# Performance work log

Hardware: AMD Instinct MI355X
Metric: run time of the kernel (lower is better)

The kernel has to match this reference:

```python
import jax, jax.numpy as jnp
import numpy as np

VOL = (32, 64, 64)          # 3D brain volume grid
B, N, D = 2, 4096, 1024     # batch, active voxels (seq_len), feature_dim
H, KNN = 16, 16             # num_heads, num_neighbors


def setup_inputs() -> dict:
    key = jax.random.key(0)
    k1, k2, k3, k4 = jax.random.split(key, 4)
    # boolean 3D mask with exactly N active voxels (so seq_len == #active)
    rng = np.random.default_rng(0)
    flat = np.zeros(int(np.prod(VOL)), dtype=bool)
    flat[rng.choice(flat.size, N, replace=False)] = True
    visual_cortex_mask = jnp.asarray(flat.reshape(VOL))
    x = jax.random.normal(k1, (B, N, D), dtype=jnp.float32)
    s = 1.0 / np.sqrt(D)
    Wq = jax.random.normal(k2, (D, D), dtype=jnp.float32) * s
    Wk = jax.random.normal(k3, (D, D), dtype=jnp.float32) * s
    Wv = jax.random.normal(k4, (D, D), dtype=jnp.float32) * s
    return {"x": x, "visual_cortex_mask": visual_cortex_mask,
            "Wq": Wq, "Wk": Wk, "Wv": Wv}


def reference(x, visual_cortex_mask, Wq, Wk, Wv):
    batch, seq_len, d = x.shape
    hd = d // H
    # --- kNN over active voxel coordinates (cdist + topk) ---
    flat = visual_cortex_mask.reshape(-1)
    (act,) = jnp.nonzero(flat, size=seq_len)  # flat indices of active voxels
    coords = jnp.stack(jnp.unravel_index(act, visual_cortex_mask.shape),
                       axis=1).astype(jnp.float32)           # [N, 3]
    sq = jnp.sum(coords * coords, axis=-1)                    # [N]
    d2 = sq[:, None] + sq[None, :] - 2.0 * (coords @ coords.T)  # squared dists
    _, nbr = jax.lax.top_k(-d2, KNN + 1)   # smallest distances first
    nbr = nbr[:, 1:]                       # drop self -> [N, KNN] positions
    # --- QKV projections (torch Linear: x @ W.T) ---
    q = (x @ Wq.T).reshape(batch, seq_len, H, hd)
    k = (x @ Wk.T).reshape(batch, seq_len, H, hd)
    v = (x @ Wv.T).reshape(batch, seq_len, H, hd)
    # --- gather-based sparse attention: each query attends only to its
    # KNN neighbors (exactly the block-mask semantics of the original) ---
    kn = k[:, nbr]   # [B, N, KNN, H, hd]
    vn = v[:, nbr]   # [B, N, KNN, H, hd]
    scale = 1.0 / np.sqrt(hd)
    scores = jnp.einsum('bnhd,bnkhd->bhnk', q, kn) * scale
    attn = jax.nn.softmax(scores, axis=-1)
    out = jnp.einsum('bhnk,bnkhd->bnhd', attn, vn).reshape(batch, seq_len, d)
    metric = k.mean(axis=2)  # key.mean over heads -> [B, N, hd]
    return out, metric
```

## Files before the change

### kernel.cpp

```cpp
#include <hip/hip_runtime.h>
#include <hip/hip_bf16.h>
#include <stdint.h>

#define BATCH 2
#define NPTS 4096
#define DMODEL 1024
#define NHEAD 16
#define HDIM 64
#define KNN 16
#define MASKN 131072
#define EBLK 128

typedef __attribute__((ext_vector_type(8))) short bf16x8;
typedef __attribute__((ext_vector_type(4))) float f32x4;

__device__ __forceinline__ float b2f(unsigned short u) {
    union { unsigned int i; float f; } c; c.i = ((unsigned int)u) << 16; return c.f;
}
__device__ __forceinline__ unsigned short f2b(float f) {
    unsigned int x = __float_as_uint(f);
    unsigned int r = (x + 0x7fffu + ((x >> 16) & 1u)) >> 16;
    return (unsigned short)r;
}
__device__ __forceinline__ unsigned int pack2f(float a, float b) {
    return (unsigned int)f2b(a) | ((unsigned int)f2b(b) << 16);
}
__device__ __forceinline__ void gload16(const unsigned short* g, unsigned short* l) {
    __builtin_amdgcn_global_load_lds((const __attribute__((address_space(1))) void*)g,
                                     (__attribute__((address_space(3))) void*)l, 16, 0, 0);
}

__global__ __launch_bounds__(256) void count8_kernel(const unsigned char* __restrict__ m8,
                                                     int* __restrict__ cnt8) {
    __shared__ int red[256];
    const int b = blockIdx.x, t = threadIdx.x;
    const uchar4 v = ((const uchar4*)m8)[b * 256 + t];
    red[t] = (v.x != 0) + (v.y != 0) + (v.z != 0) + (v.w != 0);
    __syncthreads();
    for (int off = 128; off >= 1; off >>= 1) {
        if (t < off) red[t] += red[t + off];
        __syncthreads();
    }
    if (t == 0) cnt8[b] = red[0];
}

__global__ __launch_bounds__(256) void count32_kernel(const unsigned char* __restrict__ m8,
                                                      const int* __restrict__ cnt8,
                                                      int* __restrict__ cnt32) {
    __shared__ int red[256];
    const int b = blockIdx.x, t = threadIdx.x;
    red[t] = (t < EBLK) ? cnt8[t] : 0;
    __syncthreads();
    for (int off = 128; off >= 1; off >>= 1) {
        if (t < off) red[t] += red[t + off];
        __syncthreads();
    }
    if (red[0] == NPTS) return;
    __syncthreads();
    const int4 v = ((const int4*)m8)[b * 256 + t];
    red[t] = (v.x != 0) + (v.y != 0) + (v.z != 0) + (v.w != 0);
    __syncthreads();
    for (int off = 128; off >= 1; off >>= 1) {
        if (t < off) red[t] += red[t + off];
        __syncthreads();
    }
    if (t == 0) cnt32[b] = red[0];
}

__global__ __launch_bounds__(256) void extract_kernel(const unsigned char* __restrict__ m8,
                                                      const int* __restrict__ cnt8,
                                                      const int* __restrict__ cnt32,
                                                      int* __restrict__ act) {
    __shared__ int sblk[EBLK];
    __shared__ int sthr[256];
    const int b = blockIdx.x, t = threadIdx.x;
    if (t < EBLK) sblk[t] = cnt8[t];
    __syncthreads();
    for (int off = 1; off < EBLK; off <<= 1) {
        int v = (t < EBLK && t >= off) ? sblk[t - off] : 0;
        __syncthreads();
        if (t < EBLK) sblk[t] += v;
        __syncthreads();
    }
    const bool bytes = (sblk[EBLK - 1] == NPTS);
    if (!bytes) {
        __syncthreads();
        if (t < EBLK) sblk[t] = cnt32[t];
        __syncthreads();
        for (int off = 1; off < EBLK; off <<= 1) {
            int v = (t < EBLK && t >= off) ? sblk[t - off] : 0;
            __syncthreads();
            if (t < EBLK) sblk[t] += v;
            __syncthreads();
        }
    }
    const int blkoff = (b == 0) ? 0 : sblk[b - 1];
    const int gbase = b * 1024 + t * 4;
    int f0, f1, f2, f3;
    if (bytes) {
        const uchar4 v = ((const uchar4*)m8)[b * 256 + t];
        f0 = v.x != 0; f1 = v.y != 0; f2 = v.z != 0; f3 = v.w != 0;
    } else {
        const int4 v = ((const int4*)m8)[b * 256 + t];
        f0 = v.x != 0; f1 = v.y != 0; f2 = v.z != 0; f3 = v.w != 0;
    }
    const int c = f0 + f1 + f2 + f3;
    sthr[t] = c;
    __syncthreads();
    for (int off = 1; off < 256; off <<= 1) {
        int v = (t >= off) ? sthr[t - off] : 0;
        __syncthreads();
        sthr[t] += v;
        __syncthreads();
    }
    int pos = blkoff + sthr[t] - c;
    if (f0) act[pos++] = gbase;
    if (f1) act[pos++] = gbase + 1;
    if (f2) act[pos++] = gbase + 2;
    if (f3) act[pos++] = gbase + 3;
}

__global__ __launch_bounds__(256) void knn_kernel(const int* __restrict__ act,
                                                  int* __restrict__ nbr) {
    __shared__ int act_s[NPTS];
    const int t = threadIdx.x;
    for (int i = t; i < NPTS; i += 256) act_s[i] = act[i];
    __syncthreads();
    const int q = blockIdx.x * 4 + (t >> 6);
    const int lane = t & 63;
    const int aq = act_s[q];
    const int qz = aq >> 12, qy = (aq >> 6) & 63, qx = aq & 63;
    int best[17];
    #pragma unroll
    for (int i = 0; i < 17; ++i) best[i] = 0x7FFFFFFF;
    for (int j = lane; j < NPTS; j += 64) {
        const int aj = act_s[j];
        const int dz = (aj >> 12) - qz;
        const int dy = ((aj >> 6) & 63) - qy;
        const int dx = (aj & 63) - qx;
        const int d2 = dz * dz + dy * dy + dx * dx;
        int p = (d2 << 12) | j;
        if (p < best[16]) {
            #pragma unroll
            for (int u = 0; u < 17; ++u) {
                const bool lt = p < best[u];
                const int tmp = best[u];
                best[u] = lt ? p : best[u];
                p = lt ? tmp : p;
            }
        }
    }
    int head = best[0];
    int keep = 0;
    #pragma unroll
    for (int r = 0; r < KNN + 1; ++r) {
        int m = head;
        #pragma unroll
        for (int off = 32; off >= 1; off >>= 1) m = min(m, __shfl_xor(m, off, 64));
        if (lane == r - 1) keep = m;
        const bool win = (head == m);
        #pragma unroll
        for (int u = 0; u < 16; ++u) if (win) best[u] = best[u + 1];
        if (win) best[16] = 0x7FFFFFFF;
        head = best[0];
    }
    if (lane < KNN) nbr[q * KNN + lane] = keep & 4095;
}

#define XN8 (BATCH * NPTS * DMODEL / 8)
#define WN8 (DMODEL * DMODEL / 8)
__global__ __launch_bounds__(256) void cast_all_kernel(
    const float* __restrict__ x, const float* __restrict__ wq,
    const float* __restrict__ wk, const float* __restrict__ wv,
    unsigned short* __restrict__ Xb, unsigned short* __restrict__ Wb) {
    const int i = blockIdx.x * 256 + threadIdx.x;
    const int total = XN8 + 3 * WN8;
    if (i >= total) return;
    const float* src;
    unsigned short* dst;
    if (i < XN8) {
        src = x + (size_t)i * 8;
        dst = Xb + (size_t)i * 8;
    } else {
        const int j = i - XN8;
        const int wsel = j >> 17;
        const int o = j & (WN8 - 1);
        src = ((wsel == 0) ? wq : (wsel == 1) ? wk : wv) + (size_t)o * 8;
        dst = Wb + ((size_t)wsel * WN8 + o) * 8;
    }
    const float4 a = ((const float4*)src)[0];
    const float4 b = ((const float4*)src)[1];
    uint4 w;
    w.x = pack2f(a.x, a.y); w.y = pack2f(a.z, a.w);
    w.z = pack2f(b.x, b.y); w.w = pack2f(b.z, b.w);
    *(uint4*)dst = w;
}

__global__ __launch_bounds__(256, 2) void gemm_qkv3(
    const unsigned short* __restrict__ Xb,
    const unsigned short* __restrict__ Wb,
    unsigned short* __restrict__ O0, unsigned short* __restrict__ O1, unsigned short* __restrict__ O2)
{
    const int K = DMODEL, N = DMODEL;
    __shared__ unsigned short As[2][128 * 32];
    __shared__ unsigned short Bs[3][2][128 * 32];
    const int tid = threadIdx.x;
    const int rowBase = blockIdx.x * 128;
    const int colBase = blockIdx.y * 128;
    const int lane = tid & 63, w = tid >> 6;
    const int wr = w >> 1, wc = w & 1;
    const int lr = lane & 15, kg = lane >> 4;

    f32x4 acc[3][4][4];
    const f32x4 zero = {0.f, 0.f, 0.f, 0.f};
    #pragma unroll
    for (int z = 0; z < 3; ++z)
        #pragma unroll
        for (int i = 0; i < 4; ++i)
            #pragma unroll
            for (int j = 0; j < 4; ++j) acc[z][i][j] = zero;

    const int srow4 = tid >> 2;
    const int xch = (tid & 3) ^ (srow4 & 3);
    const unsigned short* agp = &Xb[(size_t)(rowBase + srow4) * K + xch * 8];
    const unsigned short* bg0 = &Wb[(size_t)(colBase + srow4) * K + xch * 8];
    const unsigned short* bg1 = bg0 + (size_t)DMODEL * DMODEL;
    const unsigned short* bg2 = bg1 + (size_t)DMODEL * DMODEL;

    #define STAGE(kt, bf) do { \
        gload16(agp + (kt) * 32,           &As[bf][w * 512]); \
        gload16(agp + 64 * K + (kt) * 32,  &As[bf][2048 + w * 512]); \
        gload16(bg0 + (kt) * 32,           &Bs[0][bf][w * 512]); \
        gload16(bg0 + 64 * K + (kt) * 32,  &Bs[0][bf][2048 + w * 512]); \
        gload16(bg1 + (kt) * 32,           &Bs[1][bf][w * 512]); \
        gload16(bg1 + 64 * K + (kt) * 32,  &Bs[1][bf][2048 + w * 512]); \
        gload16(bg2 + (kt) * 32,           &Bs[2][bf][w * 512]); \
        gload16(bg2 + 64 * K + (kt) * 32,  &Bs[2][bf][2048 + w * 512]); \
    } while (0)

    const int rchunk = (kg ^ (lr & 3)) * 8;

    #define COMPUTE(bf) do { \
        bf16x8 af[4]; \
        _Pragma("unroll") \
        for (int mi = 0; mi < 4; ++mi) \
            af[mi] = *(const bf16x8*)&As[bf][(wr * 64 + mi * 16 + lr) * 32 + rchunk]; \
        _Pragma("unroll") \
        for (int z = 0; z < 3; ++z) { \
            bf16x8 bfr[4]; \
            _Pragma("unroll") \
            for (int ni = 0; ni < 4; ++ni) \
                bfr[ni] = *(const bf16x8*)&Bs[z][bf][(wc * 64 + ni * 16 + lr) * 32 + rchunk]; \
            __builtin_amdgcn_s_setprio(1); \
            _Pragma("unroll") \
            for (int mi = 0; mi < 4; ++mi) \
                _Pragma("unroll") \
                for (int ni = 0; ni < 4; ++ni) \
                    acc[z][mi][ni] = __builtin_amdgcn_mfma_f32_16x16x32_bf16(af[mi], bfr[ni], acc[z][mi][ni], 0, 0, 0); \
            __builtin_amdgcn_s_setprio(0); \
        } \
    } while (0)

    STAGE(0, 0);
    STAGE(1, 1);
    for (int kt = 0; kt < 30; ++kt) {
        const int bf = kt & 1;
        asm volatile("s_waitcnt vmcnt(8)" ::: "memory");
        __builtin_amdgcn_s_barrier();
        COMPUTE(bf);
        __builtin_amdgcn_s_barrier();
        STAGE(kt + 2, bf);
    }
    asm volatile("s_waitcnt vmcnt(8)" ::: "memory");
    __builtin_amdgcn_s_barrier();
    COMPUTE(0);
    __builtin_amdgcn_s_barrier();
    asm volatile("s_waitcnt vmcnt(0)" ::: "memory");
    __builtin_amdgcn_s_barrier();
    COMPUTE(1);
    #undef STAGE
    #undef COMPUTE

    #pragma unroll
    for (int z = 0; z < 3; ++z) {
        unsigned short* C = (z == 0) ? O0 : (z == 1) ? O1 : O2;
        #pragma unroll
        for (int mi = 0; mi < 4; ++mi)
            #pragma unroll
            for (int ni = 0; ni < 4; ++ni) {
                const int row0 = rowBase + wr * 64 + mi * 16 + kg * 4;
                const int col = colBase + wc * 64 + ni * 16 + lr;
                #pragma unroll
                for (int j = 0; j < 4; ++j)
                    C[(size_t)(row0 + j) * N + col] = f2b(acc[z][mi][ni][j]);
            }
    }
}

__device__ __forceinline__ void stage16(unsigned short* dst, const float* src) {
    const float4 a = ((const float4*)src)[0];
    const float4 b = ((const float4*)src)[1];
    const float4 c = ((const float4*)src)[2];
    const float4 d = ((const float4*)src)[3];
    uint4 w0, w1;
    w0.x = pack2f(a.x, a.y); w0.y = pack2f(a.z, a.w);
    w0.z = pack2f(b.x, b.y); w0.w = pack2f(b.z, b.w);
    w1.x = pack2f(c.x, c.y); w1.y = pack2f(c.z, c.w);
    w1.z = pack2f(d.x, d.y); w1.w = pack2f(d.z, d.w);
    ((uint4*)dst)[0] = w0;
    ((uint4*)dst)[1] = w1;
}

__global__ __launch_bounds__(256) void gemm_qkv_f32(
    const float* __restrict__ X,
    const float* __restrict__ W0, const float* __restrict__ W1, const float* __restrict__ W2,
    unsigned short* __restrict__ O0, unsigned short* __restrict__ O1, unsigned short* __restrict__ O2)
{
    const int K = DMODEL, N = DMODEL;
    const float* W = (blockIdx.z == 0) ? W0 : (blockIdx.z == 1) ? W1 : W2;
    unsigned short* C = (blockIdx.z == 0) ? O0 : (blockIdx.z == 1) ? O1 : O2;
    __shared__ unsigned short As[128 * 32];
    __shared__ unsigned short Bs[128 * 32];
    const int tid = threadIdx.x;
    const int rowBase = blockIdx.x * 128;
    const int colBase = blockIdx.y * 128;
    const int lane = tid & 63, w = tid >> 6;
    const int wr = w >> 1, wc = w & 1;
    const int lr = lane & 15, kg = lane >> 4;
    const int srow = tid >> 1;
    const int scol = (tid & 1) * 16;
    f32x4 acc[4][4];
    const f32x4 zero = {0.f, 0.f, 0.f, 0.f};
    #pragma unroll
    for (int i = 0; i < 4; ++i)
        #pragma unroll
        for (int j = 0; j < 4; ++j) acc[i][j] = zero;
    const float* Arow = &X[(size_t)(rowBase + srow) * K + scol];
    const float* Brow = &W[(size_t)(colBase + srow) * K + scol];
    unsigned short* Adst = &As[srow * 32 + scol];
    unsigned short* Bdst = &Bs[srow * 32 + scol];
    for (int kb = 0; kb < K; kb += 32) {
        __syncthreads();
        stage16(Adst, Arow + kb);
        stage16(Bdst, Brow + kb);
        __syncthreads();
        bf16x8 af[4], bfr[4];
        #pragma unroll
        for (int mi = 0; mi < 4; ++mi)
            af[mi] = *(const bf16x8*)&As[(wr * 64 + mi * 16 + lr) * 32 + kg * 8];
        #pragma unroll
        for (int ni = 0; ni < 4; ++ni)
            bfr[ni] = *(const bf16x8*)&Bs[(wc * 64 + ni * 16 + lr) * 32 + kg * 8];
        #pragma unroll
        for (int mi = 0; mi < 4; ++mi)
            #pragma unroll
            for (int ni = 0; ni < 4; ++ni)
                acc[mi][ni] = __builtin_amdgcn_mfma_f32_16x16x32_bf16(af[mi], bfr[ni], acc[mi][ni], 0, 0, 0);
    }
    #pragma unroll
    for (int mi = 0; mi < 4; ++mi)
        #pragma unroll
        for (int ni = 0; ni < 4; ++ni) {
            const int row0 = rowBase + wr * 64 + mi * 16 + kg * 4;
            const int col = colBase + wc * 64 + ni * 16 + lr;
            #pragma unroll
            for (int j = 0; j < 4; ++j)
                C[(size_t)(row0 + j) * N + col] = f2b(acc[mi][ni][j]);
        }
}

__global__ __launch_bounds__(256) void attn_kernel(
    const unsigned short* __restrict__ Q, const unsigned short* __restrict__ Kb,
    const unsigned short* __restrict__ Vb, const int* __restrict__ nbr,
    float* __restrict__ out, float* __restrict__ mout)
{
    const int bid = blockIdx.x;
    const int p = (bid & 7) * 1024 + (bid >> 3);
    const int b = p >> 12;
    const int n = p & 4095;
    __shared__ unsigned short q_s[DMODEL];
    __shared__ float a_s[NHEAD][KNN];
    __shared__ float part_s[4][64];
    const int tid = threadIdx.x;
    const int kk = tid & 15, h = tid >> 4;
    const int mynb = nbr[n * KNN + kk];
    const unsigned short* krow = &Kb[((size_t)b * NPTS + mynb) * DMODEL + h * HDIM];
    bf16x8 kreg[8];
    #pragma unroll
    for (int j = 0; j < 8; ++j) kreg[j] = *(const bf16x8*)&krow[j * 8];
    const int o = tid * 4;
    ushort4 vpre[KNN];
    #pragma unroll
    for (int k2 = 0; k2 < KNN; ++k2) {
        const int nb2 = __shfl(mynb, k2, 16);
        vpre[k2] = *(const ushort4*)&Vb[((size_t)b * NPTS + nb2) * DMODEL + o];
    }
    *(int2*)&q_s[tid * 4] = *(const int2*)&Q[((size_t)b * NPTS + n) * DMODEL + tid * 4];
    __syncthreads();
    float s = 0.f;
    #pragma unroll
    for (int j = 0; j < 8; ++j) {
        const bf16x8 qq = *(const bf16x8*)&q_s[h * HDIM + j * 8];
        const bf16x8 kr = kreg[j];
        #pragma unroll
        for (int e = 0; e < 8; ++e)
            s += b2f((unsigned short)qq[e]) * b2f((unsigned short)kr[e]);
    }
    s *= 0.125f;
    float m = s;
    #pragma unroll
    for (int off = 8; off >= 1; off >>= 1) m = fmaxf(m, __shfl_xor(m, off, 16));
    const float e = __expf(s - m);
    float sum = e;
    #pragma unroll
    for (int off = 8; off >= 1; off >>= 1) sum += __shfl_xor(sum, off, 16);
    a_s[h][kk] = e / sum;
    __syncthreads();
    const int h2 = tid >> 4;
    float av0 = 0.f, av1 = 0.f, av2 = 0.f, av3 = 0.f;
    #pragma unroll
    for (int k2 = 0; k2 < KNN; ++k2) {
        const float a = a_s[h2][k2];
        av0 += a * b2f(vpre[k2].x); av1 += a * b2f(vpre[k2].y);
        av2 += a * b2f(vpre[k2].z); av3 += a * b2f(vpre[k2].w);
    }
    float4 r; r.x = av0; r.y = av1; r.z = av2; r.w = av3;
    *(float4*)&out[((size_t)b * NPTS + n) * DMODEL + o] = r;
    {
        const unsigned short* krow2 = &Kb[((size_t)b * NPTS + n) * DMODEL];
        const int dd = tid & 63, grp = tid >> 6;
        float ms = 0.f;
        #pragma unroll
        for (int hh = 0; hh < 4; ++hh)
            ms += b2f(krow2[(grp * 4 + hh) * HDIM + dd]);
        part_s[grp][dd] = ms;
        __syncthreads();
        if (tid < 64)
            mout[((size_t)b * NPTS + n) * HDIM + tid] =
                (part_s[0][tid] + part_s[1][tid] + part_s[2][tid] + part_s[3][tid]) * 0.0625f;
    }
}

extern "C" void kernel_launch(void* const* d_in, const int* in_sizes, int n_in,
                              void* d_out, int out_size, void* d_ws, size_t ws_size,
                              hipStream_t stream) {
    const float* x = (const float*)d_in[0];
    const unsigned char* mask = (const unsigned char*)d_in[1];
    const float* Wq = (const float*)d_in[2];
    const float* Wk = (const float*)d_in[3];
    const float* Wv = (const float*)d_in[4];
    float* out = (float*)d_out;
    char* ws = (char*)d_ws;

    const size_t QKV_BYTES = (size_t)BATCH * NPTS * DMODEL * 2;
    const size_t XB_BYTES  = (size_t)BATCH * NPTS * DMODEL * 2;
    const size_t WB_BYTES  = (size_t)3 * DMODEL * DMODEL * 2;
    unsigned short* qb = (unsigned short*)(ws);
    unsigned short* kb = (unsigned short*)(ws + QKV_BYTES);
    unsigned short* vb = (unsigned short*)(ws + 2 * QKV_BYTES);
    const size_t SMALL_BYTES = (size_t)NPTS * sizeof(int) * (1 + KNN) + 2 * EBLK * sizeof(int);
    const size_t need_base = 3 * QKV_BYTES + SMALL_BYTES;
    const size_t need_full = need_base + XB_BYTES + WB_BYTES;
    const bool full = (ws_size >= need_full);
    char* tail = ws + 3 * QKV_BYTES;
    unsigned short* Xb = (unsigned short*)tail;
    unsigned short* Wb = (unsigned short*)(tail + XB_BYTES);
    char* small = full ? (tail + XB_BYTES + WB_BYTES) : tail;
    int* act  = (int*)small;
    int* nbr  = (int*)(small + NPTS * sizeof(int));
    int* cnt8 = (int*)(small + NPTS * sizeof(int) * (1 + KNN));
    int* cnt32 = cnt8 + EBLK;
    if (ws_size < need_base) return;

    count8_kernel<<<EBLK, 256, 0, stream>>>(mask, cnt8);
    count32_kernel<<<EBLK, 256, 0, stream>>>(mask, cnt8, cnt32);
    extract_kernel<<<EBLK, 256, 0, stream>>>(mask, cnt8, cnt32, act);
    knn_kernel<<<1024, 256, 0, stream>>>(act, nbr);
    if (full) {
        const int castN = XN8 + 3 * WN8;
        cast_all_kernel<<<(castN + 255) / 256, 256, 0, stream>>>(x, Wq, Wk, Wv, Xb, Wb);
        gemm_qkv3<<<dim3(64, 8), 256, 0, stream>>>(Xb, Wb, qb, kb, vb);
    } else {
        gemm_qkv_f32<<<dim3(64, 8, 3), 256, 0, stream>>>(x, Wq, Wk, Wv, qb, kb, vb);
    }
    attn_kernel<<<dim3(BATCH * NPTS), 256, 0, stream>>>(qb, kb, vb, nbr, out,
                                                        out + (size_t)BATCH * NPTS * DMODEL);
}
```

Baseline: 173.5 us.

## Split fused QKV GEMM into per-matrix blocks with 64-wide K tiles

The fused kernel that computed Q, K and V in one block (three accumulator sets, 32-wide K tiles) is replaced by a kernel launched over a grid z-dimension of 3, each block computing one projection with a 64-wide K step and an XOR swizzle over 8 chunks. This cuts accumulator registers and LDS per block, allows more blocks (512 to 1536) to fill the CUs, and halves the number of barrier-separated k-iterations. In exchange, each X tile is loaded three times instead of once.

```diff
diff --git a/kernel.cpp b/kernel.cpp
--- a/kernel.cpp
+++ b/kernel.cpp
@@ -196,14 +196,16 @@
     *(uint4*)dst = w;
 }
 
-__global__ __launch_bounds__(256, 2) void gemm_qkv3(
+__global__ __launch_bounds__(256, 2) void gemm_qkv64(
     const unsigned short* __restrict__ Xb,
     const unsigned short* __restrict__ Wb,
     unsigned short* __restrict__ O0, unsigned short* __restrict__ O1, unsigned short* __restrict__ O2)
 {
     const int K = DMODEL, N = DMODEL;
-    __shared__ unsigned short As[2][128 * 32];
-    __shared__ unsigned short Bs[3][2][128 * 32];
+    const unsigned short* W = Wb + (size_t)blockIdx.z * DMODEL * DMODEL;
+    unsigned short* C = (blockIdx.z == 0) ? O0 : (blockIdx.z == 1) ? O1 : O2;
+    __shared__ unsigned short As[2][128 * 64];
+    __shared__ unsigned short Bs[2][128 * 64];
     const int tid = threadIdx.x;
     const int rowBase = blockIdx.x * 128;
     const int colBase = blockIdx.y * 128;
@@ -211,59 +213,58 @@
     const int wr = w >> 1, wc = w & 1;
     const int lr = lane & 15, kg = lane >> 4;
 
-    f32x4 acc[3][4][4];
+    f32x4 acc[4][4];
     const f32x4 zero = {0.f, 0.f, 0.f, 0.f};
     #pragma unroll
-    for (int z = 0; z < 3; ++z)
-        #pragma unroll
-        for (int i = 0; i < 4; ++i)
-            #pragma unroll
-            for (int j = 0; j < 4; ++j) acc[z][i][j] = zero;
-
-    const int srow4 = tid >> 2;
-    const int xch = (tid & 3) ^ (srow4 & 3);
-    const unsigned short* agp = &Xb[(size_t)(rowBase + srow4) * K + xch * 8];
-    const unsigned short* bg0 = &Wb[(size_t)(colBase + srow4) * K + xch * 8];
-    const unsigned short* bg1 = bg0 + (size_t)DMODEL * DMODEL;
-    const unsigned short* bg2 = bg1 + (size_t)DMODEL * DMODEL;
+    for (int i = 0; i < 4; ++i)
+        #pragma unroll
+        for (int j = 0; j < 4; ++j) acc[i][j] = zero;
+
+    const unsigned short* aS[4];
+    const unsigned short* bS[4];
+    #pragma unroll
+    for (int j = 0; j < 4; ++j) {
+        const int s = j * 256 + tid;
+        const int row = s >> 3, pch = s & 7;
+        const int sc = (pch ^ (row & 7)) * 8;
+        aS[j] = Xb + (size_t)(rowBase + row) * K + sc;
+        bS[j] = W  + (size_t)(colBase + row) * K + sc;
+    }
 
     #define STAGE(kt, bf) do { \
-        gload16(agp + (kt) * 32,           &As[bf][w * 512]); \
-        gload16(agp + 64 * K + (kt) * 32,  &As[bf][2048 + w * 512]); \
-        gload16(bg0 + (kt) * 32,           &Bs[0][bf][w * 512]); \
-        gload16(bg0 + 64 * K + (kt) * 32,  &Bs[0][bf][2048 + w * 512]); \
-        gload16(bg1 + (kt) * 32,           &Bs[1][bf][w * 512]); \
-        gload16(bg1 + 64 * K + (kt) * 32,  &Bs[1][bf][2048 + w * 512]); \
-        gload16(bg2 + (kt) * 32,           &Bs[2][bf][w * 512]); \
-        gload16(bg2 + 64 * K + (kt) * 32,  &Bs[2][bf][2048 + w * 512]); \
+        _Pragma("unroll") \
+        for (int j = 0; j < 4; ++j) { \
+            gload16(aS[j] + (kt) * 64, &As[bf][(j * 256 + w * 64) * 8]); \
+            gload16(bS[j] + (kt) * 64, &Bs[bf][(j * 256 + w * 64) * 8]); \
+        } \
     } while (0)
 
-    const int rchunk = (kg ^ (lr & 3)) * 8;
-
     #define COMPUTE(bf) do { \
-        bf16x8 af[4]; \
+        bf16x8 af[4][2], bfr[4][2]; \
         _Pragma("unroll") \
         for (int mi = 0; mi < 4; ++mi) \
-            af[mi] = *(const bf16x8*)&As[bf][(wr * 64 + mi * 16 + lr) * 32 + rchunk]; \
+            _Pragma("unroll") \
+            for (int kk = 0; kk < 2; ++kk) \
+                af[mi][kk] = *(const bf16x8*)&As[bf][(wr * 64 + mi * 16 + lr) * 64 + (((kk * 4 + kg) ^ (lr & 7)) * 8)]; \
         _Pragma("unroll") \
-        for (int z = 0; z < 3; ++z) { \
-            bf16x8 bfr[4]; \
+        for (int ni = 0; ni < 4; ++ni) \
             _Pragma("unroll") \
-            for (int ni = 0; ni < 4; ++ni) \
-                bfr[ni] = *(const bf16x8*)&Bs[z][bf][(wc * 64 + ni * 16 + lr) * 32 + rchunk]; \
-            __builtin_amdgcn_s_setprio(1); \
+            for (int kk = 0; kk < 2; ++kk) \
+                bfr[ni][kk] = *(const bf16x8*)&Bs[bf][(wc * 64 + ni * 16 + lr) * 64 + (((kk * 4 + kg) ^ (lr & 7)) * 8)]; \
+        __builtin_amdgcn_s_setprio(1); \
+        _Pragma("unroll") \
+        for (int kk = 0; kk < 2; ++kk) \
             _Pragma("unroll") \
             for (int mi = 0; mi < 4; ++mi) \
                 _Pragma("unroll") \
                 for (int ni = 0; ni < 4; ++ni) \
-                    acc[z][mi][ni] = __builtin_amdgcn_mfma_f32_16x16x32_bf16(af[mi], bfr[ni], acc[z][mi][ni], 0, 0, 0); \
-            __builtin_amdgcn_s_setprio(0); \
-        } \
+                    acc[mi][ni] = __builtin_amdgcn_mfma_f32_16x16x32_bf16(af[mi][kk], bfr[ni][kk], acc[mi][ni], 0, 0, 0); \
+        __builtin_amdgcn_s_setprio(0); \
     } while (0)
 
     STAGE(0, 0);
     STAGE(1, 1);
-    for (int kt = 0; kt < 30; ++kt) {
+    for (int kt = 0; kt < 14; ++kt) {
         const int bf = kt & 1;
         asm volatile("s_waitcnt vmcnt(8)" ::: "memory");
         __builtin_amdgcn_s_barrier();
@@ -282,19 +283,15 @@
     #undef COMPUTE
 
     #pragma unroll
-    for (int z = 0; z < 3; ++z) {
-        unsigned short* C = (z == 0) ? O0 : (z == 1) ? O1 : O2;
-        #pragma unroll
-        for (int mi = 0; mi < 4; ++mi)
+    for (int mi = 0; mi < 4; ++mi)
+        #pragma unroll
+        for (int ni = 0; ni < 4; ++ni) {
+            const int row0 = rowBase + wr * 64 + mi * 16 + kg * 4;
+            const int col = colBase + wc * 64 + ni * 16 + lr;
             #pragma unroll
-            for (int ni = 0; ni < 4; ++ni) {
-                const int row0 = rowBase + wr * 64 + mi * 16 + kg * 4;
-                const int col = colBase + wc * 64 + ni * 16 + lr;
-                #pragma unroll
-                for (int j = 0; j < 4; ++j)
-                    C[(size_t)(row0 + j) * N + col] = f2b(acc[z][mi][ni][j]);
-            }
-    }
+            for (int j = 0; j < 4; ++j)
+                C[(size_t)(row0 + j) * N + col] = f2b(acc[mi][ni][j]);
+        }
 }
 
 __device__ __forceinline__ void stage16(unsigned short* dst, const float* src) {
@@ -479,7 +476,7 @@
     if (full) {
         const int castN = XN8 + 3 * WN8;
         cast_all_kernel<<<(castN + 255) / 256, 256, 0, stream>>>(x, Wq, Wk, Wv, Xb, Wb);
-        gemm_qkv3<<<dim3(64, 8), 256, 0, stream>>>(Xb, Wb, qb, kb, vb);
+        gemm_qkv64<<<dim3(64, 8, 3), 256, 0, stream>>>(Xb, Wb, qb, kb, vb);
     } else {
         gemm_qkv_f32<<<dim3(64, 8, 3), 256, 0, stream>>>(x, Wq, Wk, Wv, qb, kb, vb);
     }
```

Measured after the change: 174.4 us. About the same (+0.5%).
